# Kernel tuning notes

Measured on AMD Instinct MI355X. Metric: run time of the kernel, lower is better.

The kernel has to match this reference:

```python
import jax, jax.numpy as jnp
import numpy as np

B, IN_DIM, T = 4, 512, 4096
EMBED, HEADS, NB_FEAT = 1024, 16, 256
D_HEAD = EMBED // HEADS
EPS = 1e-6


def _orthogonal_random_matrix(key, nb_rows, nb_cols):
    # scaling==1 branch: sqrt(nb_cols) * Q from reduced QR of a Gaussian block
    block = jax.random.normal(key, (nb_rows, nb_cols), dtype=jnp.float32)
    q, _ = jnp.linalg.qr(block)
    return jnp.sqrt(jnp.float32(nb_cols)) * q


def setup_inputs() -> dict:
    key = jax.random.key(0)
    kx, kq, kk, kv, ko, kp = jax.random.split(key, 6)
    s = 1.0 / np.sqrt(IN_DIM)
    return {
        "x": jax.random.normal(kx, (B, IN_DIM, T), dtype=jnp.float32),
        "Wq": jax.random.normal(kq, (IN_DIM, EMBED), dtype=jnp.float32) * s,
        "Wk": jax.random.normal(kk, (IN_DIM, EMBED), dtype=jnp.float32) * s,
        "Wv": jax.random.normal(kv, (IN_DIM, EMBED), dtype=jnp.float32) * s,
        "Wo": jax.random.normal(ko, (EMBED, EMBED), dtype=jnp.float32) * (1.0 / np.sqrt(EMBED)),
        "proj": _orthogonal_random_matrix(kp, NB_FEAT, D_HEAD),
    }


def reference(x, Wq, Wk, Wv, Wo, proj):
    b, c, t = x.shape
    x_bt = jnp.transpose(x, (0, 2, 1))  # (B, T, in_dim)
    Q = (x_bt @ Wq).reshape(b, t, HEADS, D_HEAD)
    K = (x_bt @ Wk).reshape(b, t, HEADS, D_HEAD)
    V = (x_bt @ Wv).reshape(b, t, HEADS, D_HEAD)
    # exponential random-feature map
    Qp = jnp.exp(jnp.einsum('bthd,fd->bthf', Q, proj)) + EPS
    Kp = jnp.exp(jnp.einsum('bthd,fd->bthf', K, proj)) + EPS
    K_sum = Kp.sum(axis=1)                              # (B, H, F)
    KV = jnp.einsum('bthf,bthd->bhfd', Kp, V)           # (B, H, F, D)
    denom = jnp.maximum(jnp.einsum('bthf,bhf->bth', Qp, K_sum), 1e-6)
    numer = jnp.einsum('bthf,bhfd->bthd', Qp, KV)
    attn = numer / denom[..., None]                     # (B, T, H, D)
    out2 = attn.reshape(b, t, HEADS * D_HEAD) @ Wo      # (B, T, embed)
    cat = jnp.concatenate([x_bt, out2], axis=-1)        # (B, T, in_dim+embed)
    return jnp.transpose(cat, (0, 2, 1))
```

## Files before the change

kernel.cpp:

```cpp
#include <hip/hip_runtime.h>


constexpr int kB  = 4;
constexpr int kIn = 512;
constexpr int kT  = 4096;
constexpr int kE  = 1024;
constexpr int kH  = 16;
constexpr int kD  = 64;
constexpr int kF  = 256;
constexpr int kQKVs = 3072;

typedef __attribute__((ext_vector_type(8))) short bf16x8;
typedef __attribute__((ext_vector_type(4))) float f32x4;

__device__ __forceinline__ unsigned short f2bf(float f) {
    unsigned u = __float_as_uint(f);
    u += 0x7fff + ((u >> 16) & 1);
    return (unsigned short)(u >> 16);
}
__device__ __forceinline__ float bf2f(unsigned short s) {
    return __uint_as_float(((unsigned)s) << 16);
}
__device__ __forceinline__ void gload_lds16(const void* g, void* l) {
    __builtin_amdgcn_global_load_lds((const __attribute__((address_space(1))) void*)g,
                                     (__attribute__((address_space(3))) void*)l, 16, 0, 0);
}

__global__ __launch_bounds__(256) void zero_kernel(float* __restrict__ p, int n) {
    int i = blockIdx.x * 256 + threadIdx.x;
    if (i < n) p[i] = 0.f;
}

__global__ __launch_bounds__(256) void copy_x_kernel(const float* __restrict__ x,
                                                     float* __restrict__ out) {
    const int perB4 = kIn * kT / 4;
    int idx = blockIdx.x * 256 + threadIdx.x;
    if (idx < kB * perB4) {
        int b = idx / perB4, e = idx % perB4;
        ((float4*)out)[(size_t)b * ((kIn + kE) * kT / 4) + e] = ((const float4*)x)[idx];
    }
}

__global__ __launch_bounds__(256) void f2b_flat_kernel(const float* __restrict__ s,
                                                       unsigned short* __restrict__ d, int n4) {
    int i = blockIdx.x * 256 + threadIdx.x;
    if (i < n4) {
        float4 v = ((const float4*)s)[i];
        ushort4 o;
        o.x = f2bf(v.x); o.y = f2bf(v.y); o.z = f2bf(v.z); o.w = f2bf(v.w);
        ((ushort4*)d)[i] = o;
    }
}

__global__ __launch_bounds__(256) void trans_f2b_kernel(const float* __restrict__ src,
                                                        unsigned short* __restrict__ dst,
                                                        int R, int C,
                                                        long sstride, long dstride) {
    __shared__ float L[64][68];
    src += (size_t)blockIdx.z * sstride;
    dst += (size_t)blockIdx.z * dstride;
    const int c0 = blockIdx.x * 64, r0 = blockIdx.y * 64;
    const int tid = threadIdx.x;
#pragma unroll
    for (int it = 0; it < 4; ++it) {
        int lin = it * 256 + tid;
        int i = lin >> 4;
        int j4 = (lin & 15) * 4;
        float4 v = *(const float4*)(src + (size_t)(r0 + i) * C + c0 + j4);
        L[j4 + 0][i] = v.x; L[j4 + 1][i] = v.y; L[j4 + 2][i] = v.z; L[j4 + 3][i] = v.w;
    }
    __syncthreads();
#pragma unroll
    for (int it = 0; it < 4; ++it) {
        int lin = it * 256 + tid;
        int cc = lin >> 4;
        int r4 = (lin & 15) * 4;
        ushort4 o;
        o.x = f2bf(L[cc][r4 + 0]); o.y = f2bf(L[cc][r4 + 1]);
        o.z = f2bf(L[cc][r4 + 2]); o.w = f2bf(L[cc][r4 + 3]);
        *(ushort4*)(dst + (size_t)(c0 + cc) * R + r0 + r4) = o;
    }
}

__global__ __launch_bounds__(256) void trans_qkv_kernel(const float* __restrict__ Wq,
                                                        const float* __restrict__ Wk,
                                                        const float* __restrict__ Wv,
                                                        unsigned short* __restrict__ dst) {
    __shared__ float L[64][68];
    const int z = blockIdx.z;
    const float* src = (z == 0) ? Wq : (z == 1) ? Wk : Wv;
    dst += (size_t)z * kE * kIn;
    const int c0 = blockIdx.x * 64, r0 = blockIdx.y * 64;
    const int tid = threadIdx.x;
#pragma unroll
    for (int it = 0; it < 4; ++it) {
        int lin = it * 256 + tid;
        int i = lin >> 4;
        int j4 = (lin & 15) * 4;
        float4 v = *(const float4*)(src + (size_t)(r0 + i) * kE + c0 + j4);
        L[j4 + 0][i] = v.x; L[j4 + 1][i] = v.y; L[j4 + 2][i] = v.z; L[j4 + 3][i] = v.w;
    }
    __syncthreads();
#pragma unroll
    for (int it = 0; it < 4; ++it) {
        int lin = it * 256 + tid;
        int cc = lin >> 4;
        int r4 = (lin & 15) * 4;
        ushort4 o;
        o.x = f2bf(L[cc][r4 + 0]); o.y = f2bf(L[cc][r4 + 1]);
        o.z = f2bf(L[cc][r4 + 2]); o.w = f2bf(L[cc][r4 + 3]);
        *(ushort4*)(dst + (size_t)(c0 + cc) * kIn + r0 + r4) = o;
    }
}

__device__ __forceinline__ void gemm128_mainloop(const unsigned short* __restrict__ A,
                                                 const unsigned short* __restrict__ Bt,
                                                 int K, int m0, int n0,
                                                 unsigned short* As, unsigned short* Bs,
                                                 f32x4 (&acc)[4][4]) {
    const int tid = threadIdx.x, lane = tid & 63, w = tid >> 6;
    const int col = lane & 15, quad = lane >> 4;
    const int wm = (w >> 2) * 64, wn = (w & 3) * 64;
    const int nt = K >> 5;

    const unsigned short* Agl  = A  + (size_t)(m0 + (tid >> 2)) * K + (tid & 3) * 8;
    const unsigned short* Bgl0 = Bt + (size_t)(n0 + (tid >> 2)) * K + (tid & 3) * 8;
    const unsigned short* Bgl1 = Bgl0 + (size_t)128 * K;
    unsigned short* Asw = As + w * 512;
    unsigned short* Bsw = Bs + w * 512;

    auto stage = [&](int kt, int buf) {
        gload_lds16(Agl  + kt * 32, Asw + buf * 4096);
        gload_lds16(Bgl0 + kt * 32, Bsw + buf * 8192);
        gload_lds16(Bgl1 + kt * 32, Bsw + buf * 8192 + 4096);
    };

#pragma unroll
    for (int i = 0; i < 4; ++i)
#pragma unroll
        for (int j = 0; j < 4; ++j) acc[i][j] = (f32x4){0.f, 0.f, 0.f, 0.f};

    stage(0, 0);
    if (nt > 1) stage(1, 1);
    asm volatile("s_waitcnt vmcnt(3)" ::: "memory");
    __builtin_amdgcn_s_barrier();
    __builtin_amdgcn_sched_barrier(0);

    for (int t = 0; t < nt; ++t) {
        const int cur = t & 1;
        const unsigned short* Ab = As + cur * 4096;
        const unsigned short* Bb = Bs + cur * 8192;
        bf16x8 av[4], bv[4];
#pragma unroll
        for (int i = 0; i < 4; ++i)
            av[i] = *(const bf16x8*)&Ab[(wm + i * 16 + col) * 32 + quad * 8];
#pragma unroll
        for (int j = 0; j < 4; ++j)
            bv[j] = *(const bf16x8*)&Bb[(wn + j * 16 + col) * 32 + quad * 8];
        asm volatile("s_waitcnt lgkmcnt(0)" ::: "memory");
        __builtin_amdgcn_sched_barrier(0);
        __builtin_amdgcn_s_barrier();
        if (t + 2 < nt) stage(t + 2, cur);
        __builtin_amdgcn_sched_barrier(0);
#pragma unroll
        for (int i = 0; i < 4; ++i)
#pragma unroll
            for (int j = 0; j < 4; ++j)
                acc[i][j] = __builtin_amdgcn_mfma_f32_16x16x32_bf16(av[i], bv[j], acc[i][j], 0, 0, 0);
        if (t + 1 < nt) {
            __builtin_amdgcn_sched_barrier(0);
            if (t + 2 < nt) asm volatile("s_waitcnt vmcnt(3)" ::: "memory");
            else            asm volatile("s_waitcnt vmcnt(0)" ::: "memory");
            __builtin_amdgcn_sched_barrier(0);
            __builtin_amdgcn_s_barrier();
            __builtin_amdgcn_sched_barrier(0);
        }
    }
}

__global__ __launch_bounds__(512, 4) void gemm128_b16(const unsigned short* __restrict__ A,
                                                      const unsigned short* __restrict__ Bt,
                                                      unsigned short* __restrict__ C,
                                                      int N, int K, int ntN) {
    __shared__ unsigned short As[2 * 4096];
    __shared__ unsigned short Bs[2 * 8192];
    __shared__ float Tt[8][336];
    const int tid = threadIdx.x, lane = tid & 63, w = tid >> 6;
    const int col = lane & 15, quad = lane >> 4;
    const int wm = (w >> 2) * 64, wn = (w & 3) * 64;
    const int bid = blockIdx.x;
    const int qch = gridDim.x >> 3;
    const int swb = (bid & 7) * qch + (bid >> 3);
    const int mt = swb / ntN, ntl = swb - mt * ntN;
    const int m0 = mt * 128, n0 = ntl * 256;

    f32x4 acc[4][4];
    gemm128_mainloop(A, Bt, K, m0, n0, As, Bs, acc);

    float* Tw = Tt[w];
    const int t2 = lane >> 2, n4 = (lane & 3) * 4;
#pragma unroll
    for (int ri = 0; ri < 4; ++ri)
#pragma unroll
        for (int cj = 0; cj < 4; ++cj) {
#pragma unroll
            for (int r = 0; r < 4; ++r)
                Tw[(quad * 4 + r) * 20 + col] = acc[ri][cj][r];
            float4 v = *(const float4*)&Tw[t2 * 20 + n4];
            ushort4 o;
            o.x = f2bf(v.x); o.y = f2bf(v.y); o.z = f2bf(v.z); o.w = f2bf(v.w);
            *(ushort4*)(C + (size_t)(m0 + wm + ri * 16 + t2) * N + n0 + wn + cj * 16 + n4) = o;
        }
}

__global__ __launch_bounds__(512, 4) void gemm128_out(const unsigned short* __restrict__ A,
                                                      const unsigned short* __restrict__ Bt,
                                                      float* __restrict__ out,
                                                      int N, int K, int ntN) {
    __shared__ unsigned short As[2 * 4096];
    __shared__ unsigned short Bs[2 * 8192];
    __shared__ float Tt[8][336];
    const int tid = threadIdx.x, lane = tid & 63, w = tid >> 6;
    const int col = lane & 15, quad = lane >> 4;
    const int wm = (w >> 2) * 64, wn = (w & 3) * 64;
    const int bid = blockIdx.x;
    const int qch = gridDim.x >> 3;
    const int swb = (bid & 7) * qch + (bid >> 3);
    const int mt = swb / ntN, ntl = swb - mt * ntN;
    const int m0 = mt * 128, n0 = ntl * 256;

    f32x4 acc[4][4];
    gemm128_mainloop(A, Bt, K, m0, n0, As, Bs, acc);

    const int b = m0 >> 12, t0 = m0 & 4095;
    float* dst = out + (size_t)b * (kIn + kE) * kT + (size_t)kIn * kT;
    float* Tw = Tt[w];
    const int n2 = lane >> 2, t4 = (lane & 3) * 4;
#pragma unroll
    for (int ri = 0; ri < 4; ++ri)
#pragma unroll
        for (int cj = 0; cj < 4; ++cj) {
            *(float4*)&Tw[col * 20 + quad * 4] =
                (float4){acc[ri][cj][0], acc[ri][cj][1], acc[ri][cj][2], acc[ri][cj][3]};
            float4 v = *(const float4*)&Tw[n2 * 20 + t4];
            *(float4*)(dst + (size_t)(n0 + wn + cj * 16 + n2) * kT + t0 + wm + ri * 16 + t4) = v;
        }
}

__global__ __launch_bounds__(256) void phaseA_mfma(const unsigned short* __restrict__ QKVb,
                                                   const unsigned short* __restrict__ projb,
                                                   float* __restrict__ KVg,
                                                   float* __restrict__ Ksumg) {
    __shared__ unsigned short Ks[64 * 64];
    __shared__ unsigned short VT[64 * 72];
    __shared__ unsigned short KpT[256 * 72];
    const int tid = threadIdx.x, lane = tid & 63, w = tid >> 6;
    const int col = lane & 15, quad = lane >> 4;
    const int bh = blockIdx.x, b = bh >> 4, h = bh & 15;
    const int grp = blockIdx.y;
    const int f0 = w * 64;
    const int swz = col & 7;

    bf16x8 bB[2][4];
#pragma unroll
    for (int s = 0; s < 2; ++s)
#pragma unroll
        for (int j = 0; j < 4; ++j)
            bB[s][j] = *(const bf16x8*)(projb + (size_t)(f0 + j * 16 + col) * 64 + s * 32 + quad * 8);

    f32x4 kvacc[4][4];
#pragma unroll
    for (int i = 0; i < 4; ++i)
#pragma unroll
        for (int j = 0; j < 4; ++j) kvacc[i][j] = (f32x4){0.f, 0.f, 0.f, 0.f};
    float ksum_acc[4] = {0.f, 0.f, 0.f, 0.f};

    for (int it = 0; it < 8; ++it) {
        const size_t rowbase = (size_t)(b * kT + grp * 512 + it * 64) * kQKVs + h * kD;
        __syncthreads();
#pragma unroll
        for (int i2 = 0; i2 < 2; ++i2) {
            int p = (i2 * 4 + w) * 64 + lane;
            int row = p >> 3;
            int cg = ((p & 7) ^ (row & 7)) * 8;
            gload_lds16(QKVb + rowbase + 1024 + (size_t)row * kQKVs + cg, &Ks[(i2 * 4 + w) * 512]);
        }
#pragma unroll
        for (int r = 0; r < 4; ++r) {
            int lin = r * 256 + tid;
            int t = lin >> 4, d4 = (lin & 15) * 4;
            ushort4 v = *(const ushort4*)(QKVb + rowbase + 2048 + (size_t)t * kQKVs + d4);
            VT[(d4 + 0) * 72 + t] = v.x; VT[(d4 + 1) * 72 + t] = v.y;
            VT[(d4 + 2) * 72 + t] = v.z; VT[(d4 + 3) * 72 + t] = v.w;
        }
        __syncthreads();
        bf16x8 av[2][4];
#pragma unroll
        for (int s = 0; s < 2; ++s)
#pragma unroll
            for (int i = 0; i < 4; ++i)
                av[s][i] = *(const bf16x8*)&Ks[(i * 16 + col) * 64 + ((s * 4 + quad) ^ swz) * 8];
#pragma unroll
        for (int j = 0; j < 4; ++j) {
            f32x4 sa[4];
#pragma unroll
            for (int i = 0; i < 4; ++i) sa[i] = (f32x4){0.f, 0.f, 0.f, 0.f};
#pragma unroll
            for (int s = 0; s < 2; ++s)
#pragma unroll
                for (int i = 0; i < 4; ++i)
                    sa[i] = __builtin_amdgcn_mfma_f32_16x16x32_bf16(av[s][i], bB[s][j], sa[i], 0, 0, 0);
            const int f = f0 + j * 16 + col;
#pragma unroll
            for (int i = 0; i < 4; ++i) {
                float e0 = __expf(sa[i][0]) + 1e-6f;
                float e1 = __expf(sa[i][1]) + 1e-6f;
                float e2 = __expf(sa[i][2]) + 1e-6f;
                float e3 = __expf(sa[i][3]) + 1e-6f;
                ksum_acc[j] += (e0 + e1) + (e2 + e3);
                ushort4 pk;
                pk.x = f2bf(e0); pk.y = f2bf(e1); pk.z = f2bf(e2); pk.w = f2bf(e3);
                *(ushort4*)&KpT[f * 72 + i * 16 + quad * 4] = pk;
            }
        }
#pragma unroll
        for (int s = 0; s < 2; ++s) {
            const int kc = s * 32 + quad * 8;
            bf16x8 a2[4], b2[4];
#pragma unroll
            for (int i = 0; i < 4; ++i)
                a2[i] = *(const bf16x8*)&KpT[(f0 + i * 16 + col) * 72 + kc];
#pragma unroll
            for (int jn = 0; jn < 4; ++jn)
                b2[jn] = *(const bf16x8*)&VT[(jn * 16 + col) * 72 + kc];
#pragma unroll
            for (int i = 0; i < 4; ++i)
#pragma unroll
                for (int jn = 0; jn < 4; ++jn)
                    kvacc[i][jn] = __builtin_amdgcn_mfma_f32_16x16x32_bf16(a2[i], b2[jn], kvacc[i][jn], 0, 0, 0);
        }
    }
    const size_t kvbase = (size_t)bh * (kF * kD);
#pragma unroll
    for (int i = 0; i < 4; ++i)
#pragma unroll
        for (int jn = 0; jn < 4; ++jn)
#pragma unroll
            for (int r = 0; r < 4; ++r)
                atomicAdd(&KVg[kvbase + (size_t)(f0 + i * 16 + quad * 4 + r) * kD + jn * 16 + col],
                          kvacc[i][jn][r]);
#pragma unroll
    for (int j = 0; j < 4; ++j) {
        float v = ksum_acc[j];
        v += __shfl_xor(v, 16);
        v += __shfl_xor(v, 32);
        if (quad == 0) atomicAdd(&Ksumg[(size_t)bh * kF + f0 + j * 16 + col], v);
    }
}

__global__ __launch_bounds__(256) void phaseB_mfma(const unsigned short* __restrict__ QKVb,
                                                   const unsigned short* __restrict__ projb,
                                                   const unsigned short* __restrict__ KVTb,
                                                   const float* __restrict__ Ksumg,
                                                   unsigned short* __restrict__ attnb) {
    __shared__ unsigned short Qs[64 * 64];
    __shared__ unsigned short Qp[64 * 264];
    __shared__ unsigned short KVTs[64 * 264];
    __shared__ float KsS[256];
    __shared__ float denp[4][64];
    const int tid = threadIdx.x, lane = tid & 63, w = tid >> 6;
    const int col = lane & 15, quad = lane >> 4;
    const int bh = blockIdx.x, b = bh >> 4, h = bh & 15;
    const int grp = blockIdx.y;
    const int f0 = w * 64;
    const int swz = col & 7;

    bf16x8 bB[2][4];
#pragma unroll
    for (int s = 0; s < 2; ++s)
#pragma unroll
        for (int j = 0; j < 4; ++j)
            bB[s][j] = *(const bf16x8*)(projb + (size_t)(f0 + j * 16 + col) * 64 + s * 32 + quad * 8);

#pragma unroll
    for (int r = 0; r < 8; ++r) {
        int lin = r * 256 + tid;
        int d = lin >> 5, fc8 = (lin & 31) * 8;
        *(bf16x8*)&KVTs[d * 264 + fc8] = *(const bf16x8*)(KVTb + (size_t)bh * 16384 + d * 256 + fc8);
    }
    KsS[tid] = Ksumg[(size_t)bh * kF + tid];

    for (int it = 0; it < 8; ++it) {
        const int tg0 = grp * 512 + it * 64;
        const size_t rowbase = (size_t)(b * kT + tg0) * kQKVs + h * kD;
        __syncthreads();
#pragma unroll
        for (int i2 = 0; i2 < 2; ++i2) {
            int p = (i2 * 4 + w) * 64 + lane;
            int row = p >> 3;
            int cg = ((p & 7) ^ (row & 7)) * 8;
            gload_lds16(QKVb + rowbase + (size_t)row * kQKVs + cg, &Qs[(i2 * 4 + w) * 512]);
        }
        __syncthreads();
        bf16x8 av[2][4];
#pragma unroll
        for (int s = 0; s < 2; ++s)
#pragma unroll
            for (int i = 0; i < 4; ++i)
                av[s][i] = *(const bf16x8*)&Qs[(i * 16 + col) * 64 + ((s * 4 + quad) ^ swz) * 8];
#pragma unroll
        for (int j = 0; j < 4; ++j) {
            f32x4 sa[4];
#pragma unroll
            for (int i = 0; i < 4; ++i) sa[i] = (f32x4){0.f, 0.f, 0.f, 0.f};
#pragma unroll
            for (int s = 0; s < 2; ++s)
#pragma unroll
                for (int i = 0; i < 4; ++i)
                    sa[i] = __builtin_amdgcn_mfma_f32_16x16x32_bf16(av[s][i], bB[s][j], sa[i], 0, 0, 0);
            const int f = f0 + j * 16 + col;
#pragma unroll
            for (int i = 0; i < 4; ++i) {
                const int tb = i * 16 + quad * 4;
                Qp[(tb + 0) * 264 + f] = f2bf(__expf(sa[i][0]) + 1e-6f);
                Qp[(tb + 1) * 264 + f] = f2bf(__expf(sa[i][1]) + 1e-6f);
                Qp[(tb + 2) * 264 + f] = f2bf(__expf(sa[i][2]) + 1e-6f);
                Qp[(tb + 3) * 264 + f] = f2bf(__expf(sa[i][3]) + 1e-6f);
            }
        }
        float dp = 0.f;
#pragma unroll
        for (int u = 0; u < 64; u += 8) {
            bf16x8 qv = *(const bf16x8*)&Qp[lane * 264 + f0 + u];
#pragma unroll
            for (int k2 = 0; k2 < 8; ++k2)
                dp += bf2f((unsigned short)qv[k2]) * KsS[f0 + u + k2];
        }
        denp[w][lane] = dp;
        __syncthreads();
        f32x4 nacc[4];
#pragma unroll
        for (int jn = 0; jn < 4; ++jn) nacc[jn] = (f32x4){0.f, 0.f, 0.f, 0.f};
#pragma unroll
        for (int s = 0; s < 8; ++s) {
            const int kc = s * 32 + quad * 8;
            bf16x8 aq = *(const bf16x8*)&Qp[(w * 16 + col) * 264 + kc];
#pragma unroll
            for (int jn = 0; jn < 4; ++jn) {
                bf16x8 bk = *(const bf16x8*)&KVTs[(jn * 16 + col) * 264 + kc];
                nacc[jn] = __builtin_amdgcn_mfma_f32_16x16x32_bf16(aq, bk, nacc[jn], 0, 0, 0);
            }
        }
#pragma unroll
        for (int r = 0; r < 4; ++r) {
            const int tl = w * 16 + quad * 4 + r;
            float den = denp[0][tl] + denp[1][tl] + denp[2][tl] + denp[3][tl];
            float rd = 1.f / fmaxf(den, 1e-6f);
            const size_t ob = (size_t)(b * kT + tg0 + tl) * kE + h * kD;
#pragma unroll
            for (int jn = 0; jn < 4; ++jn)
                attnb[ob + jn * 16 + col] = f2bf(nacc[jn][r] * rd);
        }
    }
}

extern "C" void kernel_launch(void* const* d_in, const int* in_sizes, int n_in,
                              void* d_out, int out_size, void* d_ws, size_t ws_size,
                              hipStream_t stream) {
    (void)in_sizes; (void)n_in; (void)out_size; (void)ws_size;
    const float* x    = (const float*)d_in[0];
    const float* Wq   = (const float*)d_in[1];
    const float* Wk   = (const float*)d_in[2];
    const float* Wv   = (const float*)d_in[3];
    const float* Wo   = (const float*)d_in[4];
    const float* proj = (const float*)d_in[5];
    float* out = (float*)d_out;

    char* ws = (char*)d_ws;
    unsigned short* QKVb  = (unsigned short*)(ws);
    unsigned short* attnb = (unsigned short*)(ws + 100663296);
    unsigned short* Abuf  = (unsigned short*)(ws + 100663296);
    unsigned short* Btqkv = (unsigned short*)(ws + 134217728);
    unsigned short* WoT   = (unsigned short*)(ws + 137363456);
    unsigned short* projb = (unsigned short*)(ws + 139460608);
    float*          KVg   = (float*)(ws + 139493376);
    float*          Ksumg = (float*)(ws + 143687680);
    unsigned short* KVTb  = (unsigned short*)(ws + 143753216);

    copy_x_kernel<<<dim3(8192), 256, 0, stream>>>(x, out);

    trans_f2b_kernel<<<dim3(64, 8, 4), 256, 0, stream>>>(x, Abuf, kIn, kT,
                                                         (long)kIn * kT, (long)kT * kIn);
    trans_qkv_kernel<<<dim3(16, 8, 3), 256, 0, stream>>>(Wq, Wk, Wv, Btqkv);
    trans_f2b_kernel<<<dim3(16, 16, 1), 256, 0, stream>>>(Wo, WoT, kE, kE, 0, 0);
    f2b_flat_kernel<<<dim3(16), 256, 0, stream>>>(proj, projb, kF * kD / 4);

    gemm128_b16<<<dim3(1536), 512, 0, stream>>>(Abuf, Btqkv, QKVb, kQKVs, kIn, 12);

    const int nz = kB * kH * kF * kD + kB * kH * kF;
    zero_kernel<<<dim3((nz + 255) / 256), 256, 0, stream>>>(KVg, nz);

    phaseA_mfma<<<dim3(64, 8), 256, 0, stream>>>(QKVb, projb, KVg, Ksumg);
    trans_f2b_kernel<<<dim3(1, 4, 64), 256, 0, stream>>>(KVg, KVTb, kF, kD,
                                                         (long)kF * kD, (long)kF * kD);
    phaseB_mfma<<<dim3(64, 8), 256, 0, stream>>>(QKVb, projb, KVTb, Ksumg, attnb);

    gemm128_out<<<dim3(512), 512, 0, stream>>>(attnb, WoT, out, kE, kE, 4);
}
```

Before: 374.2 us.

## Store GEMM LDS tiles fragment-contiguous and reuse A buffer for epilogue

The GEMM mainloop now places rows in shared memory so that each wave's 16x32 MFMA fragment is contiguous, indexed as lane*8. The fragment loads become linear 16-byte reads with no strided row pattern, which targets LDS bank conflicts. The separate epilogue transpose scratch is dropped and the As buffer is reused in its place. This cuts shared memory per block and may allow more resident blocks. Reusing As is safe only because every wave has passed the last mainloop barrier before the epilogue writes to it.

```diff
diff --git a/kernel.cpp b/kernel.cpp
--- a/kernel.cpp
+++ b/kernel.cpp
@@ -119,20 +119,23 @@
                                                  unsigned short* As, unsigned short* Bs,
                                                  f32x4 (&acc)[4][4]) {
     const int tid = threadIdx.x, lane = tid & 63, w = tid >> 6;
-    const int col = lane & 15, quad = lane >> 4;
-    const int wm = (w >> 2) * 64, wn = (w & 3) * 64;
     const int nt = K >> 5;
 
-    const unsigned short* Agl  = A  + (size_t)(m0 + (tid >> 2)) * K + (tid & 3) * 8;
-    const unsigned short* Bgl0 = Bt + (size_t)(n0 + (tid >> 2)) * K + (tid & 3) * 8;
-    const unsigned short* Bgl1 = Bgl0 + (size_t)128 * K;
+    const int lrow = lane & 15, lchk = lane >> 4;
+    const unsigned short* Agl =
+        A + (size_t)(m0 + (w >> 2) * 64 + (w & 3) * 16 + lrow) * K + lchk * 8;
+    const unsigned short* Bgl0 =
+        Bt + (size_t)(n0 + (w >> 2) * 64 + (w & 3) * 16 + lrow) * K + lchk * 8;
+    const unsigned short* Bgl1 =
+        Bt + (size_t)(n0 + ((w >> 2) + 2) * 64 + (w & 3) * 16 + lrow) * K + lchk * 8;
     unsigned short* Asw = As + w * 512;
-    unsigned short* Bsw = Bs + w * 512;
+    unsigned short* Bsw0 = Bs + w * 512;
+    unsigned short* Bsw1 = Bs + (w + 8) * 512;
 
     auto stage = [&](int kt, int buf) {
-        gload_lds16(Agl  + kt * 32, Asw + buf * 4096);
-        gload_lds16(Bgl0 + kt * 32, Bsw + buf * 8192);
-        gload_lds16(Bgl1 + kt * 32, Bsw + buf * 8192 + 4096);
+        gload_lds16(Agl  + kt * 32, Asw  + buf * 4096);
+        gload_lds16(Bgl0 + kt * 32, Bsw0 + buf * 8192);
+        gload_lds16(Bgl1 + kt * 32, Bsw1 + buf * 8192);
     };
 
 #pragma unroll
@@ -146,17 +149,18 @@
     __builtin_amdgcn_s_barrier();
     __builtin_amdgcn_sched_barrier(0);
 
+    const unsigned short* Afb = As + ((w >> 2) * 4) * 512 + lane * 8;
+    const unsigned short* Bfb = Bs + ((w & 3) * 4) * 512 + lane * 8;
+
     for (int t = 0; t < nt; ++t) {
         const int cur = t & 1;
-        const unsigned short* Ab = As + cur * 4096;
-        const unsigned short* Bb = Bs + cur * 8192;
         bf16x8 av[4], bv[4];
 #pragma unroll
         for (int i = 0; i < 4; ++i)
-            av[i] = *(const bf16x8*)&Ab[(wm + i * 16 + col) * 32 + quad * 8];
+            av[i] = *(const bf16x8*)(Afb + cur * 4096 + i * 512);
 #pragma unroll
         for (int j = 0; j < 4; ++j)
-            bv[j] = *(const bf16x8*)&Bb[(wn + j * 16 + col) * 32 + quad * 8];
+            bv[j] = *(const bf16x8*)(Bfb + cur * 8192 + j * 512);
         asm volatile("s_waitcnt lgkmcnt(0)" ::: "memory");
         __builtin_amdgcn_sched_barrier(0);
         __builtin_amdgcn_s_barrier();
@@ -184,7 +188,6 @@
                                                       int N, int K, int ntN) {
     __shared__ unsigned short As[2 * 4096];
     __shared__ unsigned short Bs[2 * 8192];
-    __shared__ float Tt[8][336];
     const int tid = threadIdx.x, lane = tid & 63, w = tid >> 6;
     const int col = lane & 15, quad = lane >> 4;
     const int wm = (w >> 2) * 64, wn = (w & 3) * 64;
@@ -197,7 +200,7 @@
     f32x4 acc[4][4];
     gemm128_mainloop(A, Bt, K, m0, n0, As, Bs, acc);
 
-    float* Tw = Tt[w];
+    float* Tw = (float*)As + w * 336;
     const int t2 = lane >> 2, n4 = (lane & 3) * 4;
 #pragma unroll
     for (int ri = 0; ri < 4; ++ri)
@@ -219,7 +222,6 @@
                                                       int N, int K, int ntN) {
     __shared__ unsigned short As[2 * 4096];
     __shared__ unsigned short Bs[2 * 8192];
-    __shared__ float Tt[8][336];
     const int tid = threadIdx.x, lane = tid & 63, w = tid >> 6;
     const int col = lane & 15, quad = lane >> 4;
     const int wm = (w >> 2) * 64, wn = (w & 3) * 64;
@@ -234,7 +236,7 @@
 
     const int b = m0 >> 12, t0 = m0 & 4095;
     float* dst = out + (size_t)b * (kIn + kE) * kT + (size_t)kIn * kT;
-    float* Tw = Tt[w];
+    float* Tw = (float*)As + w * 336;
     const int n2 = lane >> 2, t4 = (lane & 3) * 4;
 #pragma unroll
     for (int ri = 0; ri < 4; ++ri)
```

New measurement: 388.7 us. 1.04x slower.
